# Optimization experiments

Measured on AMD Instinct MI355X. Metric: run time of the kernel, lower is better.

The kernel has to match this reference:

```python
import jax, jax.numpy as jnp
import numpy as np

F_FRAMES = 4        # frame + 1
C_FEAT = 128        # feature_dim
H_BEV, W_BEV = 256, 256
N_AGENTS = 5        # sum(record_len)
DECAY = 0.5


def setup_inputs() -> dict:
    key = jax.random.key(0)
    k1, k2 = jax.random.split(key, 2)
    history_data = jax.random.normal(k1, (F_FRAMES, N_AGENTS, C_FEAT, H_BEV, W_BEV), dtype=jnp.float32)
    mlp_w = jax.random.normal(k2, (1, C_FEAT), dtype=jnp.float32) * (1.0 / np.sqrt(C_FEAT))
    mlp_b = jnp.zeros((1,), dtype=jnp.float32)
    record_len = jnp.array([3, 2], dtype=jnp.int32)  # static per-sample agent counts
    return {"history_data": history_data, "mlp_w": mlp_w, "mlp_b": mlp_b, "record_len": record_len}


def _history_weight(n_frames):
    w = DECAY ** jnp.arange(n_frames, dtype=jnp.float32)
    return jax.nn.softmax(w)  # matches F.softmax(decay**i, dim=0)


def _chunk_score(feat, mlp_w, mlp_b):
    # feat: [L, C, H, W] -> overall_score: [L, 1, H, W]
    L, C, H, W = feat.shape
    if L == 1:
        return jnp.ones((1, 1, H, W), feat.dtype)
    nf = feat.transpose(2, 3, 0, 1).reshape(H * W, L, C)  # '(h w) l c'
    ego = nf[:, :1, :]                                    # [HW, 1, C]
    nb = nf[:, 1:, :]                                     # [HW, L-1, C]
    q = jnp.broadcast_to(ego, nb.shape)                   # ego repeated L-1 times
    scale = 1.0 / np.sqrt(C)
    score = jnp.einsum('blc,bmc->blm', q, nb) * scale      # [HW, L-1, L-1]
    attn = jax.nn.softmax(score, axis=-1)
    ctx = jnp.einsum('blm,bmc->blc', attn, nb)             # [HW, L-1, C]
    s = jax.nn.sigmoid(ctx @ mlp_w.T + mlp_b)              # [HW, L-1, 1]
    overall = jnp.concatenate([jnp.ones((H * W, 1, 1), feat.dtype), s], axis=1)  # [HW, L, 1]
    return overall.transpose(1, 2, 0).reshape(L, 1, H, W)


def reference(history_data, mlp_w, mlp_b, record_len):
    # record_len is static metadata (torch.tensor_split uses host values)
    rl = np.asarray(record_len)
    offs = np.concatenate([[0], np.cumsum(rl)])
    n_frames = history_data.shape[0]
    hw = _history_weight(n_frames)
    masks = []
    for j in range(len(rl)):
        acc = None
        for i in range(n_frames):
            feat = history_data[i, offs[j]:offs[j + 1]]  # [L_j, C, H, W]
            s = _chunk_score(feat, mlp_w, mlp_b) * hw[i]
            acc = s if acc is None else acc + s
        # torch code thresholds at literal 0.5 (not self.threshold)
        masks.append(jnp.where(acc > 0.5, 1.0, 0.0).astype(history_data.dtype))
    mask = jnp.concatenate(masks, axis=0)  # [N, 1, H, W]
    # max_pool2d kernel 3, stride 1, padding 1
    return jax.lax.reduce_window(mask, -jnp.inf, jax.lax.max,
                                 (1, 1, 3, 3), (1, 1, 1, 1),
                                 [(0, 0), (0, 0), (1, 1), (1, 1)])
```

## Files before the change

kernel.cpp:

```cpp
#include <hip/hip_runtime.h>
#include <math.h>

#define HW_PIX 65536
#define H_BEV 256
#define W_BEV 256
#define C_FEAT 128
#define F_FRAMES 4
#define N_AGENTS 5

__device__ __forceinline__ double hist_weight(int i) {
    const double e0 = exp(1.0);
    const double e1 = exp(0.5);
    const double e2 = exp(0.25);
    const double e3 = exp(0.125);
    const double s = e0 + e1 + e2 + e3;
    double v = (i == 0) ? e0 : (i == 1) ? e1 : (i == 2) ? e2 : e3;
    return v / s;
}

__global__ __launch_bounds__(256) void score_kernel(
        const float* __restrict__ hist, const float* __restrict__ mlp_w,
        const float* __restrict__ mlp_b, float* __restrict__ ws) {
    const int fc = blockIdx.y;
    const int frame = fc >> 1;
    const int chunk = fc & 1;
    const int p = (blockIdx.x * blockDim.x + threadIdx.x) << 2;

    const float* base = hist + (size_t)frame * N_AGENTS * C_FEAT * HW_PIX;
    const double hwq = hist_weight(frame);
    const double bias = (double)mlp_b[0];
    float* outp = ws + (size_t)fc * HW_PIX + p;

    if (chunk == 0) {
        const float* a0 = base + (size_t)0 * C_FEAT * HW_PIX + p;
        const float* a1 = base + (size_t)1 * C_FEAT * HW_PIX + p;
        const float* a2 = base + (size_t)2 * C_FEAT * HW_PIX + p;
        double d1[4] = {0, 0, 0, 0}, d2[4] = {0, 0, 0, 0};
        double q1[4] = {0, 0, 0, 0}, q2[4] = {0, 0, 0, 0};
        #pragma unroll 8
        for (int c = 0; c < C_FEAT; ++c) {
            const float4 e  = *(const float4*)(a0 + (size_t)c * HW_PIX);
            const float4 n1 = *(const float4*)(a1 + (size_t)c * HW_PIX);
            const float4 n2 = *(const float4*)(a2 + (size_t)c * HW_PIX);
            const double wc = (double)mlp_w[c];
            const float* ev  = &e.x;
            const float* n1v = &n1.x;
            const float* n2v = &n2.x;
            #pragma unroll
            for (int k = 0; k < 4; ++k) {
                d1[k] += (double)ev[k] * (double)n1v[k];
                d2[k] += (double)ev[k] * (double)n2v[k];
                q1[k] += wc * (double)n1v[k];
                q2[k] += wc * (double)n2v[k];
            }
        }
        const double scale = 0.08838834764831844506;
        #pragma unroll
        for (int k = 0; k < 4; ++k) {
            double x1 = d1[k] * scale, x2 = d2[k] * scale;
            double m = fmax(x1, x2);
            double e1 = exp(x1 - m), e2 = exp(x2 - m);
            double inv = 1.0 / (e1 + e2);
            double ctxw = (e1 * q1[k] + e2 * q2[k]) * inv + bias;
            double s = 1.0 / (1.0 + exp(-ctxw));
            outp[k] = (float)(hwq * s);
        }
    } else {
        const float* a4 = base + (size_t)4 * C_FEAT * HW_PIX + p;
        double q[4] = {0, 0, 0, 0};
        #pragma unroll 8
        for (int c = 0; c < C_FEAT; ++c) {
            const float4 n = *(const float4*)(a4 + (size_t)c * HW_PIX);
            const double wc = (double)mlp_w[c];
            const float* nv = &n.x;
            #pragma unroll
            for (int k = 0; k < 4; ++k) q[k] += wc * (double)nv[k];
        }
        #pragma unroll
        for (int k = 0; k < 4; ++k) {
            double s = 1.0 / (1.0 + exp(-(q[k] + bias)));
            outp[k] = (float)(hwq * s);
        }
    }
}

__global__ __launch_bounds__(256) void mask_kernel(
        const float* __restrict__ planes, float* __restrict__ mask) {
    const int p = blockIdx.x * blockDim.x + threadIdx.x;
    if (p >= HW_PIX) return;
    #pragma unroll
    for (int j = 0; j < 2; ++j) {
        double acc = 0.0;
        #pragma unroll
        for (int i = 0; i < F_FRAMES; ++i)
            acc += (double)planes[(size_t)(i * 2 + j) * HW_PIX + p];
        mask[(size_t)j * HW_PIX + p] = (acc > 0.5) ? 1.0f : 0.0f;
    }
}

__global__ __launch_bounds__(256) void pool_kernel(
        const float* __restrict__ mask, float* __restrict__ out) {
    const int p = blockIdx.x * blockDim.x + threadIdx.x;
    if (p >= HW_PIX) return;
    const int y = p >> 8, x = p & 255;
    float m[2];
    #pragma unroll
    for (int j = 0; j < 2; ++j) {
        float mx = 0.0f;
        for (int dy = -1; dy <= 1; ++dy) {
            int yy = y + dy;
            if (yy < 0 || yy >= H_BEV) continue;
            for (int dx = -1; dx <= 1; ++dx) {
                int xx = x + dx;
                if (xx < 0 || xx >= W_BEV) continue;
                mx = fmaxf(mx, mask[(size_t)j * HW_PIX + (yy << 8) + xx]);
            }
        }
        m[j] = mx;
    }
    out[(size_t)0 * HW_PIX + p] = 1.0f;
    out[(size_t)1 * HW_PIX + p] = m[0];
    out[(size_t)2 * HW_PIX + p] = m[0];
    out[(size_t)3 * HW_PIX + p] = 1.0f;
    out[(size_t)4 * HW_PIX + p] = m[1];
}

extern "C" void kernel_launch(void* const* d_in, const int* in_sizes, int n_in,
                              void* d_out, int out_size, void* d_ws, size_t ws_size,
                              hipStream_t stream) {
    const float* hist  = (const float*)d_in[0];
    const float* mlp_w = (const float*)d_in[1];
    const float* mlp_b = (const float*)d_in[2];
    float* ws   = (float*)d_ws;
    float* mask = ws + (size_t)8 * HW_PIX;
    float* out  = (float*)d_out;

    dim3 g1(HW_PIX / (4 * 256), 8);
    score_kernel<<<g1, 256, 0, stream>>>(hist, mlp_w, mlp_b, ws);
    mask_kernel<<<HW_PIX / 256, 256, 0, stream>>>(ws, mask);
    pool_kernel<<<HW_PIX / 256, 256, 0, stream>>>(mask, out);
}
```

Measured before the change: 848.5 us.

## Split channel reduction across blocks and merge agent chunks into one pass

The score kernel is replaced by a dot kernel that splits the 128-channel reduction into four slices per frame. Each thread accumulates all five per-pixel dot products (two attention dots and three MLP projections) across all agents in one loop. Partial double-precision sums go to workspace, and the mask kernel reduces them and applies softmax, sigmoid and the frame weighting. This doubles the block count and evens out per-block work, which previously differed between the two agent chunks. The cost is extra workspace traffic for the partials.

```diff
diff --git a/kernel.cpp b/kernel.cpp
--- a/kernel.cpp
+++ b/kernel.cpp
@@ -7,95 +7,109 @@
 #define C_FEAT 128
 #define F_FRAMES 4
 #define N_AGENTS 5
+#define CSPLIT 4
+#define CCHUNK (C_FEAT / CSPLIT)
+
+struct d4 { double x, y, z, w; };
+
+__device__ __forceinline__ void fma4(d4& a, const float4 u, const float4 v) {
+    a.x += (double)u.x * (double)v.x;
+    a.y += (double)u.y * (double)v.y;
+    a.z += (double)u.z * (double)v.z;
+    a.w += (double)u.w * (double)v.w;
+}
+__device__ __forceinline__ void fma4s(d4& a, const double w, const float4 v) {
+    a.x += w * (double)v.x;
+    a.y += w * (double)v.y;
+    a.z += w * (double)v.z;
+    a.w += w * (double)v.w;
+}
 
 __device__ __forceinline__ double hist_weight(int i) {
-    const double e0 = exp(1.0);
-    const double e1 = exp(0.5);
-    const double e2 = exp(0.25);
-    const double e3 = exp(0.125);
+    const double e0 = exp(1.0), e1 = exp(0.5), e2 = exp(0.25), e3 = exp(0.125);
     const double s = e0 + e1 + e2 + e3;
     double v = (i == 0) ? e0 : (i == 1) ? e1 : (i == 2) ? e2 : e3;
     return v / s;
 }
 
-__global__ __launch_bounds__(256) void score_kernel(
+__global__ __launch_bounds__(256) void dot_kernel(
         const float* __restrict__ hist, const float* __restrict__ mlp_w,
-        const float* __restrict__ mlp_b, float* __restrict__ ws) {
-    const int fc = blockIdx.y;
-    const int frame = fc >> 1;
-    const int chunk = fc & 1;
+        double* __restrict__ part) {
+    const int fs = blockIdx.y;
+    const int frame = fs >> 2;
+    const int split = fs & 3;
     const int p = (blockIdx.x * blockDim.x + threadIdx.x) << 2;
+    const int c0 = split * CCHUNK;
 
-    const float* base = hist + (size_t)frame * N_AGENTS * C_FEAT * HW_PIX;
-    const double hwq = hist_weight(frame);
-    const double bias = (double)mlp_b[0];
-    float* outp = ws + (size_t)fc * HW_PIX + p;
+    const float* base = hist + (size_t)frame * N_AGENTS * C_FEAT * HW_PIX
+                             + (size_t)c0 * HW_PIX + p;
+    const float* a0 = base;
+    const float* a1 = base + (size_t)1 * C_FEAT * HW_PIX;
+    const float* a2 = base + (size_t)2 * C_FEAT * HW_PIX;
+    const float* a4 = base + (size_t)4 * C_FEAT * HW_PIX;
 
-    if (chunk == 0) {
-        const float* a0 = base + (size_t)0 * C_FEAT * HW_PIX + p;
-        const float* a1 = base + (size_t)1 * C_FEAT * HW_PIX + p;
-        const float* a2 = base + (size_t)2 * C_FEAT * HW_PIX + p;
-        double d1[4] = {0, 0, 0, 0}, d2[4] = {0, 0, 0, 0};
-        double q1[4] = {0, 0, 0, 0}, q2[4] = {0, 0, 0, 0};
-        #pragma unroll 8
-        for (int c = 0; c < C_FEAT; ++c) {
-            const float4 e  = *(const float4*)(a0 + (size_t)c * HW_PIX);
-            const float4 n1 = *(const float4*)(a1 + (size_t)c * HW_PIX);
-            const float4 n2 = *(const float4*)(a2 + (size_t)c * HW_PIX);
-            const double wc = (double)mlp_w[c];
-            const float* ev  = &e.x;
-            const float* n1v = &n1.x;
-            const float* n2v = &n2.x;
-            #pragma unroll
-            for (int k = 0; k < 4; ++k) {
-                d1[k] += (double)ev[k] * (double)n1v[k];
-                d2[k] += (double)ev[k] * (double)n2v[k];
-                q1[k] += wc * (double)n1v[k];
-                q2[k] += wc * (double)n2v[k];
-            }
-        }
-        const double scale = 0.08838834764831844506;
-        #pragma unroll
-        for (int k = 0; k < 4; ++k) {
-            double x1 = d1[k] * scale, x2 = d2[k] * scale;
-            double m = fmax(x1, x2);
-            double e1 = exp(x1 - m), e2 = exp(x2 - m);
-            double inv = 1.0 / (e1 + e2);
-            double ctxw = (e1 * q1[k] + e2 * q2[k]) * inv + bias;
-            double s = 1.0 / (1.0 + exp(-ctxw));
-            outp[k] = (float)(hwq * s);
-        }
-    } else {
-        const float* a4 = base + (size_t)4 * C_FEAT * HW_PIX + p;
-        double q[4] = {0, 0, 0, 0};
-        #pragma unroll 8
-        for (int c = 0; c < C_FEAT; ++c) {
-            const float4 n = *(const float4*)(a4 + (size_t)c * HW_PIX);
-            const double wc = (double)mlp_w[c];
-            const float* nv = &n.x;
-            #pragma unroll
-            for (int k = 0; k < 4; ++k) q[k] += wc * (double)nv[k];
-        }
-        #pragma unroll
-        for (int k = 0; k < 4; ++k) {
-            double s = 1.0 / (1.0 + exp(-(q[k] + bias)));
-            outp[k] = (float)(hwq * s);
-        }
+    d4 d1 = {0, 0, 0, 0}, d2 = {0, 0, 0, 0};
+    d4 q1 = {0, 0, 0, 0}, q2 = {0, 0, 0, 0}, q4 = {0, 0, 0, 0};
+
+    #pragma unroll 4
+    for (int c = 0; c < CCHUNK; ++c) {
+        const float4 e  = *(const float4*)(a0 + (size_t)c * HW_PIX);
+        const float4 n1 = *(const float4*)(a1 + (size_t)c * HW_PIX);
+        const float4 n2 = *(const float4*)(a2 + (size_t)c * HW_PIX);
+        const float4 n4 = *(const float4*)(a4 + (size_t)c * HW_PIX);
+        const double wc = (double)mlp_w[c0 + c];
+        fma4(d1, e, n1);
+        fma4(d2, e, n2);
+        fma4s(q1, wc, n1);
+        fma4s(q2, wc, n2);
+        fma4s(q4, wc, n4);
     }
+
+    double* pb = part + ((size_t)fs * 5) * HW_PIX + p;
+    *(double2*)(pb + 0 * HW_PIX)     = make_double2(d1.x, d1.y);
+    *(double2*)(pb + 0 * HW_PIX + 2) = make_double2(d1.z, d1.w);
+    *(double2*)(pb + 1 * HW_PIX)     = make_double2(d2.x, d2.y);
+    *(double2*)(pb + 1 * HW_PIX + 2) = make_double2(d2.z, d2.w);
+    *(double2*)(pb + 2 * HW_PIX)     = make_double2(q1.x, q1.y);
+    *(double2*)(pb + 2 * HW_PIX + 2) = make_double2(q1.z, q1.w);
+    *(double2*)(pb + 3 * HW_PIX)     = make_double2(q2.x, q2.y);
+    *(double2*)(pb + 3 * HW_PIX + 2) = make_double2(q2.z, q2.w);
+    *(double2*)(pb + 4 * HW_PIX)     = make_double2(q4.x, q4.y);
+    *(double2*)(pb + 4 * HW_PIX + 2) = make_double2(q4.z, q4.w);
 }
 
 __global__ __launch_bounds__(256) void mask_kernel(
-        const float* __restrict__ planes, float* __restrict__ mask) {
+        const double* __restrict__ part, const float* __restrict__ mlp_b,
+        float* __restrict__ mask) {
     const int p = blockIdx.x * blockDim.x + threadIdx.x;
     if (p >= HW_PIX) return;
+    const double bias = (double)mlp_b[0];
+    const double scale = 0.08838834764831844506;
+    double acc0 = 0.0, acc1 = 0.0;
     #pragma unroll
-    for (int j = 0; j < 2; ++j) {
-        double acc = 0.0;
+    for (int f = 0; f < F_FRAMES; ++f) {
+        double d1 = 0, d2 = 0, q1 = 0, q2 = 0, q4 = 0;
         #pragma unroll
-        for (int i = 0; i < F_FRAMES; ++i)
-            acc += (double)planes[(size_t)(i * 2 + j) * HW_PIX + p];
-        mask[(size_t)j * HW_PIX + p] = (acc > 0.5) ? 1.0f : 0.0f;
+        for (int s = 0; s < CSPLIT; ++s) {
+            const double* pp = part + ((size_t)(f * CSPLIT + s) * 5) * HW_PIX + p;
+            d1 += pp[0 * HW_PIX];
+            d2 += pp[1 * HW_PIX];
+            q1 += pp[2 * HW_PIX];
+            q2 += pp[3 * HW_PIX];
+            q4 += pp[4 * HW_PIX];
+        }
+        double x1 = d1 * scale, x2 = d2 * scale;
+        double m = fmax(x1, x2);
+        double e1 = exp(x1 - m), e2 = exp(x2 - m);
+        double ctxw = (e1 * q1 + e2 * q2) / (e1 + e2) + bias;
+        double s0 = 1.0 / (1.0 + exp(-ctxw));
+        double s1 = 1.0 / (1.0 + exp(-(q4 + bias)));
+        double hwf = hist_weight(f);
+        acc0 += hwf * s0;
+        acc1 += hwf * s1;
     }
+    mask[p]          = (acc0 > 0.5) ? 1.0f : 0.0f;
+    mask[HW_PIX + p] = (acc1 > 0.5) ? 1.0f : 0.0f;
 }
 
 __global__ __launch_bounds__(256) void pool_kernel(
@@ -131,12 +145,12 @@
     const float* hist  = (const float*)d_in[0];
     const float* mlp_w = (const float*)d_in[1];
     const float* mlp_b = (const float*)d_in[2];
-    float* ws   = (float*)d_ws;
-    float* mask = ws + (size_t)8 * HW_PIX;
-    float* out  = (float*)d_out;
+    double* part = (double*)d_ws;
+    float*  mask = (float*)(part + (size_t)16 * 5 * HW_PIX);
+    float*  out  = (float*)d_out;
 
-    dim3 g1(HW_PIX / (4 * 256), 8);
-    score_kernel<<<g1, 256, 0, stream>>>(hist, mlp_w, mlp_b, ws);
-    mask_kernel<<<HW_PIX / 256, 256, 0, stream>>>(ws, mask);
+    dim3 g1(HW_PIX / (4 * 256), F_FRAMES * CSPLIT);
+    dot_kernel<<<g1, 256, 0, stream>>>(hist, mlp_w, part);
+    mask_kernel<<<HW_PIX / 256, 256, 0, stream>>>(part, mlp_b, mask);
     pool_kernel<<<HW_PIX / 256, 256, 0, stream>>>(mask, out);
 }
```

New measurement: 841.0 us. Within noise of the previous version (-0.9%).
